# Kernel optimization log

Hardware: AMD Instinct MI355X
Metric: run time of the kernel (lower is better)

## Reference

```python
import jax, jax.numpy as jnp
import numpy as np

W = 512  # imgSize
B = 32

def setup_inputs() -> dict:
    key = jax.random.key(0)
    input_diffgrid = jax.random.normal(key, (B, 2, W, W), dtype=jnp.float32)
    return {"input_diffgrid": input_diffgrid}

def reference(input_diffgrid) -> jnp.ndarray:
    # conv_transpose2d with ones kernel (1,1,1,W) then crop [0:W] along width
    # == cumulative sum along width; likewise (1,1,W,1) == cumsum along height.
    x = jnp.cumsum(input_diffgrid[:, 0], axis=-1)  # [B, W, W], cumsum over width
    y = jnp.cumsum(input_diffgrid[:, 1], axis=-2)  # [B, W, W], cumsum over height
    return jnp.stack((x, y), axis=1)  # [B, 2, W, W]
```

## Files before the change

### kernel.cpp

```cpp
#include <hip/hip_runtime.h>

#define IMG_W 512
#define NB 32

__device__ __forceinline__ void row_cumsum_wave(const float* __restrict__ in,
                                                float* __restrict__ out,
                                                int gwave) {
    const int lane = threadIdx.x & 63;
    const int b = gwave >> 9;
    const int row = gwave & 511;
    const long base = ((long)(b * 2 + 0) * IMG_W + row) * IMG_W;

    float carry = 0.f;
#pragma unroll
    for (int it = 0; it < 2; ++it) {
        const int e = it * 256 + lane * 4;
        const float4 v = *reinterpret_cast<const float4*>(in + base + e);
        const float c0 = v.x;
        const float c1 = c0 + v.y;
        const float c2 = c1 + v.z;
        const float c3 = c2 + v.w;
        float t = c3;
#pragma unroll
        for (int d = 1; d < 64; d <<= 1) {
            const float u = __shfl_up(t, d);
            if (lane >= d) t += u;
        }
        const float excl = (t - c3) + carry;
        float4 o;
        o.x = excl + c0;
        o.y = excl + c1;
        o.z = excl + c2;
        o.w = excl + c3;
        *reinterpret_cast<float4*>(out + base + e) = o;
        carry += __shfl(t, 63);
    }
}


template <int S>
__global__ __launch_bounds__(256) void k1_fused(const float* __restrict__ in,
                                                float* __restrict__ out,
                                                float* __restrict__ ws,
                                                int xblocks) {
    if ((int)blockIdx.x < xblocks) {
        const int gwave = blockIdx.x * 4 + (threadIdx.x >> 6);
        row_cumsum_wave(in, out, gwave);
    } else {
        constexpr int ROWS = IMG_W / S;
        int yb = blockIdx.x - xblocks;
        const int s = yb % S;
        const int g = (yb / S) & 1;
        const int b = yb / (2 * S);
        const int col = g * 256 + threadIdx.x;
        const long ibase = ((long)(b * 2 + 1) * IMG_W + (long)s * ROWS) * IMG_W + col;
        float acc = 0.f;
#pragma unroll
        for (int r = 0; r < ROWS; ++r) acc += in[ibase + (long)r * IMG_W];
        ws[((long)b * S + s) * IMG_W + col] = acc;
    }
}

template <int S>
__global__ __launch_bounds__(256) void k2_scan(const float* __restrict__ in,
                                               float* __restrict__ out,
                                               const float* __restrict__ ws) {
    constexpr int ROWS = IMG_W / S;
    const int yb = blockIdx.x;
    const int s = yb % S;
    const int g = (yb / S) & 1;
    const int b = yb / (2 * S);
    const int col = g * 256 + threadIdx.x;

    float acc = 0.f;
    for (int t = 0; t < s; ++t) acc += ws[((long)b * S + t) * IMG_W + col];

    const long ibase = ((long)(b * 2 + 1) * IMG_W + (long)s * ROWS) * IMG_W + col;
#pragma unroll 8
    for (int r = 0; r < ROWS; ++r) {
        acc += in[ibase + (long)r * IMG_W];
        out[ibase + (long)r * IMG_W] = acc;
    }
}

template <int S>
static void launch_impl(const float* in, float* out, float* ws, hipStream_t stream) {
    const int xblocks = (NB * IMG_W) / 4;
    const int yblocks = NB * 2 * S;
    k1_fused<S><<<xblocks + yblocks, 256, 0, stream>>>(in, out, ws, xblocks);
    k2_scan<S><<<yblocks, 256, 0, stream>>>(in, out, ws);
}

extern "C" void kernel_launch(void* const* d_in, const int* in_sizes, int n_in,
                              void* d_out, int out_size, void* d_ws, size_t ws_size,
                              hipStream_t stream) {
    const float* in = (const float*)d_in[0];
    float* out = (float*)d_out;
    float* ws = (float*)d_ws;

    const size_t per_seg = (size_t)NB * IMG_W * sizeof(float);
    if (ws_size >= 16 * per_seg)      launch_impl<16>(in, out, ws, stream);
    else if (ws_size >= 8 * per_seg)  launch_impl<8>(in, out, ws, stream);
    else if (ws_size >= 4 * per_seg)  launch_impl<4>(in, out, ws, stream);
    else if (ws_size >= 2 * per_seg)  launch_impl<2>(in, out, ws, stream);
    else                              launch_impl<1>(in, out, ws, stream);
}
```

Baseline: 114.7 us.

## Vectorize column scan with float4, reorder blocks, interleave row-scan shuffles

The column (height) cumsum path now has each thread handle four adjacent columns with float4 loads and stores, so k2 uses 128-thread blocks covering a full row width. The partial-sum blocks are placed ahead of the row-scan blocks in the fused first kernel, which lets the long-latency column reductions start first. The row scan loads both halves at once and interleaves their two shuffle scans to expose more ILP. The segment count S rises to 32 when workspace allows, and the S=1..4 fallbacks are dropped because S/2 would break for S=1.

```diff
diff --git a/kernel.cpp b/kernel.cpp
--- a/kernel.cpp
+++ b/kernel.cpp
@@ -11,30 +11,28 @@
     const int row = gwave & 511;
     const long base = ((long)(b * 2 + 0) * IMG_W + row) * IMG_W;
 
-    float carry = 0.f;
+    const float4 va = *reinterpret_cast<const float4*>(in + base + lane * 4);
+    const float4 vb = *reinterpret_cast<const float4*>(in + base + 256 + lane * 4);
+
+    const float a0 = va.x, a1 = a0 + va.y, a2 = a1 + va.z, a3 = a2 + va.w;
+    const float b0 = vb.x, b1 = b0 + vb.y, b2 = b1 + vb.z, b3 = b2 + vb.w;
+
+    float ta = a3, tb = b3;
 #pragma unroll
-    for (int it = 0; it < 2; ++it) {
-        const int e = it * 256 + lane * 4;
-        const float4 v = *reinterpret_cast<const float4*>(in + base + e);
-        const float c0 = v.x;
-        const float c1 = c0 + v.y;
-        const float c2 = c1 + v.z;
-        const float c3 = c2 + v.w;
-        float t = c3;
-#pragma unroll
-        for (int d = 1; d < 64; d <<= 1) {
-            const float u = __shfl_up(t, d);
-            if (lane >= d) t += u;
-        }
-        const float excl = (t - c3) + carry;
-        float4 o;
-        o.x = excl + c0;
-        o.y = excl + c1;
-        o.z = excl + c2;
-        o.w = excl + c3;
-        *reinterpret_cast<float4*>(out + base + e) = o;
-        carry += __shfl(t, 63);
+    for (int d = 1; d < 64; d <<= 1) {
+        const float ua = __shfl_up(ta, d);
+        const float ub = __shfl_up(tb, d);
+        if (lane >= d) { ta += ua; tb += ub; }
     }
+    const float totalA = __shfl(ta, 63);
+    const float exA = ta - a3;
+    const float exB = totalA + (tb - b3);
+
+    float4 oa, ob;
+    oa.x = exA + a0; oa.y = exA + a1; oa.z = exA + a2; oa.w = exA + a3;
+    ob.x = exB + b0; ob.y = exB + b1; ob.z = exB + b2; ob.w = exB + b3;
+    *reinterpret_cast<float4*>(out + base + lane * 4) = oa;
+    *reinterpret_cast<float4*>(out + base + 256 + lane * 4) = ob;
 }
 
 
@@ -42,53 +40,59 @@
 __global__ __launch_bounds__(256) void k1_fused(const float* __restrict__ in,
                                                 float* __restrict__ out,
                                                 float* __restrict__ ws,
-                                                int xblocks) {
-    if ((int)blockIdx.x < xblocks) {
-        const int gwave = blockIdx.x * 4 + (threadIdx.x >> 6);
+                                                int yblocksA) {
+    constexpr int ROWS = IMG_W / S;
+    if ((int)blockIdx.x < yblocksA) {
+        const int yb = blockIdx.x;
+        const int b = yb / (S / 2);
+        const int sp = yb % (S / 2);
+        const int s = sp * 2 + (threadIdx.x >> 7);
+        const int grp = threadIdx.x & 127;
+        const long ibase = ((long)(b * 2 + 1) * IMG_W + (long)s * ROWS) * IMG_W + grp * 4;
+        float4 acc = make_float4(0.f, 0.f, 0.f, 0.f);
+#pragma unroll
+        for (int r = 0; r < ROWS; ++r) {
+            const float4 v = *reinterpret_cast<const float4*>(in + ibase + (long)r * IMG_W);
+            acc.x += v.x; acc.y += v.y; acc.z += v.z; acc.w += v.w;
+        }
+        *reinterpret_cast<float4*>(ws + ((long)b * S + s) * IMG_W + grp * 4) = acc;
+    } else {
+        const int gwave = (blockIdx.x - yblocksA) * 4 + (threadIdx.x >> 6);
         row_cumsum_wave(in, out, gwave);
-    } else {
-        constexpr int ROWS = IMG_W / S;
-        int yb = blockIdx.x - xblocks;
-        const int s = yb % S;
-        const int g = (yb / S) & 1;
-        const int b = yb / (2 * S);
-        const int col = g * 256 + threadIdx.x;
-        const long ibase = ((long)(b * 2 + 1) * IMG_W + (long)s * ROWS) * IMG_W + col;
-        float acc = 0.f;
-#pragma unroll
-        for (int r = 0; r < ROWS; ++r) acc += in[ibase + (long)r * IMG_W];
-        ws[((long)b * S + s) * IMG_W + col] = acc;
     }
 }
 
 template <int S>
-__global__ __launch_bounds__(256) void k2_scan(const float* __restrict__ in,
+__global__ __launch_bounds__(128) void k2_scan(const float* __restrict__ in,
                                                float* __restrict__ out,
                                                const float* __restrict__ ws) {
     constexpr int ROWS = IMG_W / S;
     const int yb = blockIdx.x;
+    const int b = yb / S;
     const int s = yb % S;
-    const int g = (yb / S) & 1;
-    const int b = yb / (2 * S);
-    const int col = g * 256 + threadIdx.x;
+    const int grp = threadIdx.x;
 
-    float acc = 0.f;
-    for (int t = 0; t < s; ++t) acc += ws[((long)b * S + t) * IMG_W + col];
+    float4 acc = make_float4(0.f, 0.f, 0.f, 0.f);
+    for (int u = 0; u < s; ++u) {
+        const float4 w = *reinterpret_cast<const float4*>(ws + ((long)b * S + u) * IMG_W + grp * 4);
+        acc.x += w.x; acc.y += w.y; acc.z += w.z; acc.w += w.w;
+    }
 
-    const long ibase = ((long)(b * 2 + 1) * IMG_W + (long)s * ROWS) * IMG_W + col;
-#pragma unroll 8
+    const long ibase = ((long)(b * 2 + 1) * IMG_W + (long)s * ROWS) * IMG_W + grp * 4;
+#pragma unroll
     for (int r = 0; r < ROWS; ++r) {
-        acc += in[ibase + (long)r * IMG_W];
-        out[ibase + (long)r * IMG_W] = acc;
+        const float4 v = *reinterpret_cast<const float4*>(in + ibase + (long)r * IMG_W);
+        acc.x += v.x; acc.y += v.y; acc.z += v.z; acc.w += v.w;
+        *reinterpret_cast<float4*>(out + ibase + (long)r * IMG_W) = acc;
     }
 }
 
 template <int S>
 static void launch_impl(const float* in, float* out, float* ws, hipStream_t stream) {
+    const int yblocksA = NB * (S / 2);
     const int xblocks = (NB * IMG_W) / 4;
-    const int yblocks = NB * 2 * S;
-    k1_fused<S><<<xblocks + yblocks, 256, 0, stream>>>(in, out, ws, xblocks);
-    k2_scan<S><<<yblocks, 256, 0, stream>>>(in, out, ws);
+    k1_fused<S><<<yblocksA + xblocks, 256, 0, stream>>>(in, out, ws, yblocksA);
+    k2_scan<S><<<NB * S, 128, 0, stream>>>(in, out, ws);
 }
 
 extern "C" void kernel_launch(void* const* d_in, const int* in_sizes, int n_in,
@@ -99,9 +103,7 @@
     float* ws = (float*)d_ws;
 
     const size_t per_seg = (size_t)NB * IMG_W * sizeof(float);
-    if (ws_size >= 16 * per_seg)      launch_impl<16>(in, out, ws, stream);
-    else if (ws_size >= 8 * per_seg)  launch_impl<8>(in, out, ws, stream);
-    else if (ws_size >= 4 * per_seg)  launch_impl<4>(in, out, ws, stream);
-    else if (ws_size >= 2 * per_seg)  launch_impl<2>(in, out, ws, stream);
-    else                              launch_impl<1>(in, out, ws, stream);
+    if (ws_size >= 32 * per_seg)      launch_impl<32>(in, out, ws, stream);
+    else if (ws_size >= 16 * per_seg) launch_impl<16>(in, out, ws, stream);
+    else                              launch_impl<8>(in, out, ws, stream);
 }
```

Measured after the change: 119.2 us. +3.9%, slower.
